# Kernel optimization log

Measured on AMD Instinct MI355X. Metric: run time of the kernel, lower is better.

The kernel has to match this reference:

```python
import jax, jax.numpy as jnp
import numpy as np

B, G, T, F_IN = 32, 128, 128, 318


def _lin(x, W, b):
    # torch Linear: y = x @ W.T + b, W: (out, in)
    return x @ W.T + b


def _sap(rep, W1, b1, W2, b2):
    # SelfAttentionPooling over second-to-last axis. rep: (..., T, H)
    s = _lin(jax.nn.relu(_lin(rep, W1, b1)), W2, b2)[..., 0]  # (..., T)
    w = jax.nn.softmax(s, axis=-1)
    return jnp.einsum('...th,...t->...h', rep, w)  # (..., H)


def setup_inputs() -> dict:
    key = jax.random.key(0)
    ks = jax.random.split(key, 20)

    def w(k, shape, fan_in):
        bound = 1.0 / np.sqrt(fan_in)
        return jax.random.uniform(k, shape, jnp.float32, -bound, bound)

    inp = {
        'x': jax.random.normal(ks[0], (B, G, T, F_IN), jnp.float32),
        # model1: 318->50->20->20
        'W1a': w(ks[1], (50, 318), 318), 'b1a': w(ks[2], (50,), 318),
        'W1b': w(ks[3], (20, 50), 50),  'b1b': w(ks[4], (20,), 50),
        'W1c': w(ks[5], (20, 20), 20),  'b1c': w(ks[6], (20,), 20),
        # model2 pooling (input_dim=20, hidden=10)
        'pW1': w(ks[7], (10, 20), 20),  'pb1': w(ks[8], (10,), 20),
        'pW2': w(ks[9], (1, 10), 10),   'pb2': w(ks[10], (1,), 10),
        # model2_1 pooling
        'qW1': w(ks[11], (10, 20), 20), 'qb1': w(ks[12], (10,), 20),
        'qW2': w(ks[13], (1, 10), 10),  'qb2': w(ks[14], (1,), 10),
        # model3: 20->10->1
        'W3a': w(ks[15], (10, 20), 20), 'b3a': w(ks[16], (10,), 20),
        'W3b': w(ks[17], (1, 10), 10),  'b3b': w(ks[18], (1,), 10),
    }
    return inp


def reference(x, W1a, b1a, W1b, b1b, W1c, b1c, pW1, pb1, pW2, pb2,
              qW1, qb1, qW2, qb2, W3a, b3a, W3b, b3b):
    # model1 MLP on features: (B,G,T,318) -> (B,G,T,20)
    h = jax.nn.relu(_lin(x, W1a, b1a))
    h = jax.nn.relu(_lin(h, W1b, b1b))
    h = jax.nn.relu(_lin(h, W1c, b1c))
    # pool over T: (B,G,20)
    r = _sap(h, pW1, pb1, pW2, pb2)
    # pool over G: (B,20)
    r = _sap(r, qW1, qb1, qW2, qb2)
    # F.normalize (L2 over dim=1, eps=1e-12)
    norm = jnp.linalg.norm(r, axis=-1, keepdims=True)
    r = r / jnp.maximum(norm, 1e-12)
    # model3: (B,1)
    out = _lin(jax.nn.relu(_lin(r, W3a, b3a)), W3b, b3b)
    return out
```

## Files before the change

kernel.cpp:

```cpp
#include <hip/hip_runtime.h>
#include <hip/hip_bf16.h>
#include <math.h>
#include <stdint.h>

typedef __attribute__((ext_vector_type(8))) short bf16x8;
typedef __attribute__((ext_vector_type(4))) float floatx4;

static __device__ __forceinline__ unsigned short f32_to_bf16_rne(float f) {
    union { float f; uint32_t u; } v; v.f = f;
    uint32_t u = v.u;
    return (unsigned short)((u + 0x7fffu + ((u >> 16) & 1u)) >> 16);
}
static __device__ __forceinline__ float bf16_to_f32(unsigned short h) {
    union { uint32_t u; float f; } v; v.u = ((uint32_t)h) << 16;
    return v.f;
}
static __device__ __forceinline__ bf16x8 cvt8(const float2* p) {
    union { __hip_bfloat162 h[4]; bf16x8 v; } u;
    #pragma unroll
    for (int j = 0; j < 4; ++j)
        u.h[j] = __float22bfloat162_rn({p[j].x, p[j].y});
    return u.v;
}

#define BAR() do { \
    asm volatile("s_waitcnt lgkmcnt(0)" ::: "memory"); \
    __builtin_amdgcn_s_barrier(); \
    asm volatile("" ::: "memory"); } while (0)

__global__ void prep_w(const float* __restrict__ W1a, unsigned short* __restrict__ Bpre) {
    int idx = blockIdx.x * 256 + threadIdx.x;
    if (idx >= 40960) return;
    int e  = idx & 7;
    int n  = (idx >> 3) & 63;
    int kq = (idx >> 9) & 3;
    int p  = (idx >> 11) & 1;
    int ks = idx >> 12;
    int k  = ks * 32 + kq * 8 + e;
    float w = (n < 50 && k < 318) ? W1a[n * 318 + k] : 0.0f;
    unsigned short hi = f32_to_bf16_rne(w);
    Bpre[idx] = (p == 0) ? hi : f32_to_bf16_rne(w - bf16_to_f32(hi));
}

#define SLAB (64 * 318)
#define H1S 52

__global__ __launch_bounds__(256, 2)
void gemm_h1(const float* __restrict__ x,
             const unsigned short* __restrict__ Bpre,
             const float* __restrict__ b1a,
             float* __restrict__ h1g)
{
    __shared__ __align__(16) char bsm[81920];

    const int tid  = threadIdx.x;
    const int wv   = tid >> 6;
    const int lane = tid & 63;
    const int fr   = lane & 15;
    const int kq   = lane >> 4;

    const float* arow = x + (size_t)blockIdx.x * SLAB + (wv * 16 + fr) * 318 + kq * 8;

    floatx4 gb[20];
    #pragma unroll
    for (int j = 0; j < 20; ++j)
        gb[j] = *(const floatx4*)((const char*)Bpre + (j * 256 + tid) * 16);

    float2 af[40];
    #pragma unroll
    for (int ks = 0; ks < 10; ++ks)
        #pragma unroll
        for (int j = 0; j < 4; ++j) {
            bool pad = (ks == 9) && (kq == 3) && (j == 3);
            af[ks * 4 + j] = pad ? make_float2(0.f, 0.f)
                                 : *(const float2*)(arow + ks * 32 + 2 * j);
        }
    __builtin_amdgcn_sched_barrier(0);

    #pragma unroll
    for (int j = 0; j < 20; ++j)
        *(floatx4*)(bsm + (j * 256 + tid) * 16) = gb[j];
    BAR();

    floatx4 acc[4];
    #pragma unroll
    for (int nf = 0; nf < 4; ++nf) acc[nf] = (floatx4){0.f, 0.f, 0.f, 0.f};

    #pragma unroll
    for (int ks = 0; ks < 10; ++ks) {
        const char* bb = bsm + ks * 8192 + (kq << 10) + (fr << 4);
        bf16x8 a = cvt8(&af[ks * 4]);
        #pragma unroll
        for (int nf = 0; nf < 4; ++nf) {
            bf16x8 bh = *(const bf16x8*)(bb + nf * 256);
            bf16x8 bl = *(const bf16x8*)(bb + 4096 + nf * 256);
            acc[nf] = __builtin_amdgcn_mfma_f32_16x16x32_bf16(a, bh, acc[nf], 0, 0, 0);
            acc[nf] = __builtin_amdgcn_mfma_f32_16x16x32_bf16(a, bl, acc[nf], 0, 0, 0);
        }
    }

    {
        float* hrow = h1g + ((size_t)blockIdx.x * 64 + wv * 16 + kq * 4) * H1S;
        #pragma unroll
        for (int nf = 0; nf < 4; ++nf) {
            int n = nf * 16 + fr;
            if (n < 50) {
                float bia = b1a[n];
                #pragma unroll
                for (int r = 0; r < 4; ++r)
                    hrow[r * H1S + n] = fmaxf(acc[nf][r] + bia, 0.0f);
            }
        }
    }
}

__global__ __launch_bounds__(256, 4)
void tail_pool(const float* __restrict__ h1g,
               const float* __restrict__ W1b, const float* __restrict__ b1b,
               const float* __restrict__ W1c, const float* __restrict__ b1c,
               const float* __restrict__ pW1, const float* __restrict__ pb1,
               const float* __restrict__ pW2, const float* __restrict__ pb2,
               float* __restrict__ partials)
{
    const int t    = blockIdx.x * 256 + threadIdx.x;
    const int lane = threadIdx.x & 63;

    float hv[52];
    {
        const float4* hr = (const float4*)(h1g + (size_t)t * H1S);
        #pragma unroll
        for (int j = 0; j < 13; ++j) {
            float4 u = hr[j];
            hv[4 * j] = u.x; hv[4 * j + 1] = u.y;
            hv[4 * j + 2] = u.z; hv[4 * j + 3] = u.w;
        }
    }

    float h2[20];
    #pragma unroll
    for (int o = 0; o < 20; ++o) h2[o] = b1b[o];
    #pragma unroll
    for (int i = 0; i < 50; ++i) {
        float hvv = hv[i];
        #pragma unroll
        for (int o = 0; o < 20; ++o) h2[o] = fmaf(hvv, W1b[o * 50 + i], h2[o]);
    }
    #pragma unroll
    for (int o = 0; o < 20; ++o) h2[o] = fmaxf(h2[o], 0.0f);

    float h3[20];
    #pragma unroll
    for (int o = 0; o < 20; ++o) {
        float a = b1c[o];
        const float* w = W1c + o * 20;
        #pragma unroll
        for (int i = 0; i < 20; ++i) a = fmaf(h2[i], w[i], a);
        h3[o] = fmaxf(a, 0.0f);
    }

    float s = pb2[0];
    #pragma unroll
    for (int j = 0; j < 10; ++j) {
        float a = pb1[j];
        const float* w = pW1 + j * 20;
        #pragma unroll
        for (int i = 0; i < 20; ++i) a = fmaf(h3[i], w[i], a);
        s = fmaf(fmaxf(a, 0.0f), pW2[j], s);
    }

    float m = s;
    #pragma unroll
    for (int d = 32; d > 0; d >>= 1) m = fmaxf(m, __shfl_xor(m, d));
    float e = expf(s - m);
    float S = e;
    #pragma unroll
    for (int d = 32; d > 0; d >>= 1) S += __shfl_xor(S, d);

    float V[20];
    #pragma unroll
    for (int o = 0; o < 20; ++o) {
        float v = e * h3[o];
        #pragma unroll
        for (int d = 32; d > 0; d >>= 1) v += __shfl_xor(v, d);
        V[o] = v;
    }

    float myv = m;
    if (lane == 1) myv = S;
    #pragma unroll
    for (int o = 0; o < 20; ++o) if (lane == o + 2) myv = V[o];
    if (lane < 22) partials[(size_t)(t >> 6) * 24 + lane] = myv;
}

__global__ __launch_bounds__(128, 4)
void pool_g_head(const float* __restrict__ partials,
                 const float* __restrict__ qW1, const float* __restrict__ qb1,
                 const float* __restrict__ qW2, const float* __restrict__ qb2,
                 const float* __restrict__ W3a, const float* __restrict__ b3a,
                 const float* __restrict__ W3b, const float* __restrict__ b3b,
                 float* __restrict__ out)
{
    __shared__ float red_m[2];
    __shared__ float red_s[2];
    __shared__ float part[2][20];

    const int tid = threadIdx.x;
    const int b = blockIdx.x;
    const float* P = partials + ((size_t)(b * 128 + tid)) * 48;

    float m0 = P[0], S0 = P[1], m1 = P[24], S1 = P[25];
    float m = fmaxf(m0, m1);
    float w0 = expf(m0 - m), w1 = expf(m1 - m);
    float den = fmaf(S0, w0, S1 * w1);

    float v[20];
    #pragma unroll
    for (int o = 0; o < 20; ++o)
        v[o] = fmaf(P[2 + o], w0, P[26 + o] * w1) / den;

    float s = qb2[0];
    #pragma unroll
    for (int j = 0; j < 10; ++j) {
        float a = qb1[j];
        const float* w = qW1 + j * 20;
        #pragma unroll
        for (int i = 0; i < 20; ++i) a = fmaf(v[i], w[i], a);
        s = fmaf(fmaxf(a, 0.0f), qW2[j], s);
    }

    const int wig = tid >> 6, lane = tid & 63;
    float mm = s;
    #pragma unroll
    for (int d = 32; d > 0; d >>= 1) mm = fmaxf(mm, __shfl_xor(mm, d));
    if (lane == 0) red_m[wig] = mm;
    __syncthreads();
    mm = fmaxf(red_m[0], red_m[1]);

    float e = expf(s - mm);
    float su = e;
    #pragma unroll
    for (int d = 32; d > 0; d >>= 1) su += __shfl_xor(su, d);
    if (lane == 0) red_s[wig] = su;

    #pragma unroll
    for (int o = 0; o < 20; ++o) {
        float val = e * v[o];
        #pragma unroll
        for (int d = 32; d > 0; d >>= 1) val += __shfl_xor(val, d);
        if (lane == 0) part[wig][o] = val;
    }
    __syncthreads();

    if (tid == 0) {
        float dg = red_s[0] + red_s[1];
        float rb[20];
        float n2 = 0.0f;
        #pragma unroll
        for (int o = 0; o < 20; ++o) {
            rb[o] = (part[0][o] + part[1][o]) / dg;
            n2 = fmaf(rb[o], rb[o], n2);
        }
        float nrm = fmaxf(sqrtf(n2), 1e-12f);
        #pragma unroll
        for (int o = 0; o < 20; ++o) rb[o] /= nrm;

        float accv = b3b[0];
        #pragma unroll
        for (int j = 0; j < 10; ++j) {
            float a = b3a[j];
            const float* w = W3a + j * 20;
            #pragma unroll
            for (int i = 0; i < 20; ++i) a = fmaf(rb[i], w[i], a);
            accv = fmaf(fmaxf(a, 0.0f), W3b[j], accv);
        }
        out[b] = accv;
    }
}

extern "C" void kernel_launch(void* const* d_in, const int* in_sizes, int n_in,
                              void* d_out, int out_size, void* d_ws, size_t ws_size,
                              hipStream_t stream) {
    const float* x   = (const float*)d_in[0];
    const float* W1a = (const float*)d_in[1];
    const float* b1a = (const float*)d_in[2];
    const float* W1b = (const float*)d_in[3];
    const float* b1b = (const float*)d_in[4];
    const float* W1c = (const float*)d_in[5];
    const float* b1c = (const float*)d_in[6];
    const float* pW1 = (const float*)d_in[7];
    const float* pb1 = (const float*)d_in[8];
    const float* pW2 = (const float*)d_in[9];
    const float* pb2 = (const float*)d_in[10];
    const float* qW1 = (const float*)d_in[11];
    const float* qb1 = (const float*)d_in[12];
    const float* qW2 = (const float*)d_in[13];
    const float* qb2 = (const float*)d_in[14];
    const float* W3a = (const float*)d_in[15];
    const float* b3a = (const float*)d_in[16];
    const float* W3b = (const float*)d_in[17];
    const float* b3b = (const float*)d_in[18];

    float* partials      = (float*)d_ws;
    unsigned short* Bpre = (unsigned short*)((char*)d_ws + 786432);
    float* h1g           = (float*)((char*)d_ws + 868352);

    prep_w<<<160, 256, 0, stream>>>(W1a, Bpre);
    gemm_h1<<<8192, 256, 0, stream>>>(x, Bpre, b1a, h1g);
    tail_pool<<<2048, 256, 0, stream>>>(
        h1g, W1b, b1b, W1c, b1c, pW1, pb1, pW2, pb2, partials);
    pool_g_head<<<32, 128, 0, stream>>>(
        partials, qW1, qb1, qW2, qb2, W3a, b3a, W3b, b3b, (float*)d_out);
}
```

Measured before the change: 242.9 us.

## Make gemm_h1 persistent over 8 slabs with double-buffered A register prefetch

Each gemm_h1 block now handles 8 consecutive 64-row slabs instead of one, so the B-matrix staging into LDS happens once per 8 slabs. Within the block, the next slab's A tile is loaded into a second register buffer while the current slab is converted to bf16 and multiplied with MFMA, overlapping global loads with compute. A is loaded as float4 and the bias is hoisted into registers. The cost is higher register pressure from two 20-float4 buffers at launch bounds (256,2), and fewer blocks (1024) to spread across the GPU.

```diff
diff --git a/kernel.cpp b/kernel.cpp
--- a/kernel.cpp
+++ b/kernel.cpp
@@ -15,11 +15,12 @@
     union { uint32_t u; float f; } v; v.u = ((uint32_t)h) << 16;
     return v.f;
 }
-static __device__ __forceinline__ bf16x8 cvt8(const float2* p) {
+static __device__ __forceinline__ bf16x8 cvt8(float4 a, float4 b) {
     union { __hip_bfloat162 h[4]; bf16x8 v; } u;
-    #pragma unroll
-    for (int j = 0; j < 4; ++j)
-        u.h[j] = __float22bfloat162_rn({p[j].x, p[j].y});
+    u.h[0] = __float22bfloat162_rn({a.x, a.y});
+    u.h[1] = __float22bfloat162_rn({a.z, a.w});
+    u.h[2] = __float22bfloat162_rn({b.x, b.y});
+    u.h[3] = __float22bfloat162_rn({b.z, b.w});
     return u.v;
 }
 
@@ -45,6 +46,42 @@
 #define SLAB (64 * 318)
 #define H1S 52
 
+#define LOADA(AF, SOFF) { \
+    const float* ap_ = abase0 + (size_t)(SOFF) * SLAB; \
+    _Pragma("unroll") for (int ks_ = 0; ks_ < 10; ++ks_) { \
+        AF[2 * ks_] = *(const float4*)(ap_ + ks_ * 32); \
+        if (ks_ == 9 && kq == 3) { \
+            float2 t_ = *(const float2*)(ap_ + 9 * 32 + 4); \
+            AF[19] = make_float4(t_.x, t_.y, 0.f, 0.f); \
+        } else { \
+            AF[2 * ks_ + 1] = *(const float4*)(ap_ + ks_ * 32 + 4); \
+        } \
+    } } \
+    __builtin_amdgcn_sched_barrier(0);
+
+#define COMPSTORE(AF, SOFF) { \
+    floatx4 acc[4]; \
+    _Pragma("unroll") for (int nf_ = 0; nf_ < 4; ++nf_) \
+        acc[nf_] = (floatx4){0.f, 0.f, 0.f, 0.f}; \
+    _Pragma("unroll") for (int ks_ = 0; ks_ < 10; ++ks_) { \
+        const char* bb_ = bsm + ks_ * 8192 + (kq << 10) + (fr << 4); \
+        bf16x8 a_ = cvt8(AF[2 * ks_], AF[2 * ks_ + 1]); \
+        _Pragma("unroll") for (int nf_ = 0; nf_ < 4; ++nf_) { \
+            bf16x8 bh_ = *(const bf16x8*)(bb_ + nf_ * 256); \
+            bf16x8 bl_ = *(const bf16x8*)(bb_ + 4096 + nf_ * 256); \
+            acc[nf_] = __builtin_amdgcn_mfma_f32_16x16x32_bf16(a_, bh_, acc[nf_], 0, 0, 0); \
+            acc[nf_] = __builtin_amdgcn_mfma_f32_16x16x32_bf16(a_, bl_, acc[nf_], 0, 0, 0); \
+        } \
+    } \
+    float* hrow_ = h1g + ((slab0 + (SOFF)) * 64 + wv * 16 + kq * 4) * H1S; \
+    _Pragma("unroll") for (int nf_ = 0; nf_ < 4; ++nf_) { \
+        int n_ = nf_ * 16 + fr; \
+        if (n_ < 50) { \
+            _Pragma("unroll") for (int r_ = 0; r_ < 4; ++r_) \
+                hrow_[r_ * H1S + n_] = fmaxf(acc[nf_][r_] + bia4[nf_], 0.0f); \
+        } \
+    } }
+
 __global__ __launch_bounds__(256, 2)
 void gemm_h1(const float* __restrict__ x,
              const unsigned short* __restrict__ Bpre,
@@ -59,58 +96,36 @@
     const int fr   = lane & 15;
     const int kq   = lane >> 4;
 
-    const float* arow = x + (size_t)blockIdx.x * SLAB + (wv * 16 + fr) * 318 + kq * 8;
+    const size_t slab0 = (size_t)blockIdx.x * 8;
+    const float* abase0 = x + slab0 * SLAB + (wv * 16 + fr) * 318 + kq * 8;
 
     floatx4 gb[20];
     #pragma unroll
     for (int j = 0; j < 20; ++j)
         gb[j] = *(const floatx4*)((const char*)Bpre + (j * 256 + tid) * 16);
 
-    float2 af[40];
-    #pragma unroll
-    for (int ks = 0; ks < 10; ++ks)
-        #pragma unroll
-        for (int j = 0; j < 4; ++j) {
-            bool pad = (ks == 9) && (kq == 3) && (j == 3);
-            af[ks * 4 + j] = pad ? make_float2(0.f, 0.f)
-                                 : *(const float2*)(arow + ks * 32 + 2 * j);
-        }
-    __builtin_amdgcn_sched_barrier(0);
+    float4 af0[20], af1[20];
+    LOADA(af0, 0);
+
+    float bia4[4];
+    #pragma unroll
+    for (int nf = 0; nf < 4; ++nf) {
+        int n = nf * 16 + fr;
+        bia4[nf] = (n < 50) ? b1a[n] : 0.0f;
+    }
 
     #pragma unroll
     for (int j = 0; j < 20; ++j)
         *(floatx4*)(bsm + (j * 256 + tid) * 16) = gb[j];
     BAR();
 
-    floatx4 acc[4];
-    #pragma unroll
-    for (int nf = 0; nf < 4; ++nf) acc[nf] = (floatx4){0.f, 0.f, 0.f, 0.f};
-
-    #pragma unroll
-    for (int ks = 0; ks < 10; ++ks) {
-        const char* bb = bsm + ks * 8192 + (kq << 10) + (fr << 4);
-        bf16x8 a = cvt8(&af[ks * 4]);
-        #pragma unroll
-        for (int nf = 0; nf < 4; ++nf) {
-            bf16x8 bh = *(const bf16x8*)(bb + nf * 256);
-            bf16x8 bl = *(const bf16x8*)(bb + 4096 + nf * 256);
-            acc[nf] = __builtin_amdgcn_mfma_f32_16x16x32_bf16(a, bh, acc[nf], 0, 0, 0);
-            acc[nf] = __builtin_amdgcn_mfma_f32_16x16x32_bf16(a, bl, acc[nf], 0, 0, 0);
-        }
-    }
-
-    {
-        float* hrow = h1g + ((size_t)blockIdx.x * 64 + wv * 16 + kq * 4) * H1S;
-        #pragma unroll
-        for (int nf = 0; nf < 4; ++nf) {
-            int n = nf * 16 + fr;
-            if (n < 50) {
-                float bia = b1a[n];
-                #pragma unroll
-                for (int r = 0; r < 4; ++r)
-                    hrow[r * H1S + n] = fmaxf(acc[nf][r] + bia, 0.0f);
-            }
-        }
+    #pragma unroll 1
+    for (int p = 0; p < 4; ++p) {
+        const int s = 2 * p;
+        LOADA(af1, s + 1);
+        COMPSTORE(af0, s);
+        if (p < 3) { LOADA(af0, s + 2); }
+        COMPSTORE(af1, s + 1);
     }
 }
 
@@ -305,7 +320,7 @@
     float* h1g           = (float*)((char*)d_ws + 868352);
 
     prep_w<<<160, 256, 0, stream>>>(W1a, Bpre);
-    gemm_h1<<<8192, 256, 0, stream>>>(x, Bpre, b1a, h1g);
+    gemm_h1<<<1024, 256, 0, stream>>>(x, Bpre, b1a, h1g);
     tail_pool<<<2048, 256, 0, stream>>>(
         h1g, W1b, b1b, W1c, b1c, pW1, pb1, pW2, pb2, partials);
     pool_g_head<<<32, 128, 0, stream>>>(
```

After: 252.5 us. +4.0%, slower.

## Pipeline x slab via async global-to-LDS loads and keep W1a fragments in registers

Applied to the files above, without the earlier changes.

The first-layer GEMM now keeps each wave's B fragments (hi/lo bf16 split) in registers and has each wave own one 16-column output tile. It no longer stages all of W1a in LDS. The 64-row x slab is streamed in four 16-row quarters through a double-buffered LDS ring filled by global_load_lds, so loads overlap with MFMA compute. LDS use shrinks and launch bounds go from 2 to 3 blocks per CU to raise occupancy. The trade-offs are more barriers, a hardcoded clamp on the end-of-buffer address, and possible LDS bank conflicts from the 1272-byte row stride.

```diff
diff --git a/kernel.cpp b/kernel.cpp
--- a/kernel.cpp
+++ b/kernel.cpp
@@ -15,18 +15,14 @@
     union { uint32_t u; float f; } v; v.u = ((uint32_t)h) << 16;
     return v.f;
 }
-static __device__ __forceinline__ bf16x8 cvt8(const float2* p) {
+static __device__ __forceinline__ bf16x8 cvt8(floatx4 a, floatx4 b) {
     union { __hip_bfloat162 h[4]; bf16x8 v; } u;
-    #pragma unroll
-    for (int j = 0; j < 4; ++j)
-        u.h[j] = __float22bfloat162_rn({p[j].x, p[j].y});
+    u.h[0] = __float22bfloat162_rn({a[0], a[1]});
+    u.h[1] = __float22bfloat162_rn({a[2], a[3]});
+    u.h[2] = __float22bfloat162_rn({b[0], b[1]});
+    u.h[3] = __float22bfloat162_rn({b[2], b[3]});
     return u.v;
 }
-
-#define BAR() do { \
-    asm volatile("s_waitcnt lgkmcnt(0)" ::: "memory"); \
-    __builtin_amdgcn_s_barrier(); \
-    asm volatile("" ::: "memory"); } while (0)
 
 __global__ void prep_w(const float* __restrict__ W1a, unsigned short* __restrict__ Bpre) {
     int idx = blockIdx.x * 256 + threadIdx.x;
@@ -42,16 +38,22 @@
     Bpre[idx] = (p == 0) ? hi : f32_to_bf16_rne(w - bf16_to_f32(hi));
 }
 
-#define SLAB (64 * 318)
-#define H1S 52
-
-__global__ __launch_bounds__(256, 2)
+#define SLABB 81408
+#define QDATA 20352
+#define QSTG  20480
+#define H1S   52
+
+#define GLL(g, l) __builtin_amdgcn_global_load_lds( \
+    (const __attribute__((address_space(1))) void*)(g), \
+    (__attribute__((address_space(3))) void*)(l), 16, 0, 0)
+
+__global__ __launch_bounds__(256, 3)
 void gemm_h1(const float* __restrict__ x,
              const unsigned short* __restrict__ Bpre,
              const float* __restrict__ b1a,
              float* __restrict__ h1g)
 {
-    __shared__ __align__(16) char bsm[81920];
+    __shared__ __align__(1024) char sbuf[2 * QSTG];
 
     const int tid  = threadIdx.x;
     const int wv   = tid >> 6;
@@ -59,59 +61,71 @@
     const int fr   = lane & 15;
     const int kq   = lane >> 4;
 
-    const float* arow = x + (size_t)blockIdx.x * SLAB + (wv * 16 + fr) * 318 + kq * 8;
-
-    floatx4 gb[20];
-    #pragma unroll
-    for (int j = 0; j < 20; ++j)
-        gb[j] = *(const floatx4*)((const char*)Bpre + (j * 256 + tid) * 16);
-
-    float2 af[40];
-    #pragma unroll
-    for (int ks = 0; ks < 10; ++ks)
-        #pragma unroll
-        for (int j = 0; j < 4; ++j) {
-            bool pad = (ks == 9) && (kq == 3) && (j == 3);
-            af[ks * 4 + j] = pad ? make_float2(0.f, 0.f)
-                                 : *(const float2*)(arow + ks * 32 + 2 * j);
+    const size_t slab = blockIdx.x;
+    const char* xs = (const char*)x + slab * SLABB;
+    const char* xclamp = (const char*)x + 666894336 - 16;
+
+    bf16x8 Bh[10], Bl[10];
+    {
+        const char* bb = (const char*)Bpre + (kq << 10) + ((wv * 16 + fr) << 4);
+        #pragma unroll
+        for (int ks = 0; ks < 10; ++ks) {
+            Bh[ks] = *(const bf16x8*)(bb + ks * 8192);
+            Bl[ks] = *(const bf16x8*)(bb + ks * 8192 + 4096);
         }
-    __builtin_amdgcn_sched_barrier(0);
-
-    #pragma unroll
-    for (int j = 0; j < 20; ++j)
-        *(floatx4*)(bsm + (j * 256 + tid) * 16) = gb[j];
-    BAR();
-
-    floatx4 acc[4];
-    #pragma unroll
-    for (int nf = 0; nf < 4; ++nf) acc[nf] = (floatx4){0.f, 0.f, 0.f, 0.f};
-
-    #pragma unroll
-    for (int ks = 0; ks < 10; ++ks) {
-        const char* bb = bsm + ks * 8192 + (kq << 10) + (fr << 4);
-        bf16x8 a = cvt8(&af[ks * 4]);
-        #pragma unroll
-        for (int nf = 0; nf < 4; ++nf) {
-            bf16x8 bh = *(const bf16x8*)(bb + nf * 256);
-            bf16x8 bl = *(const bf16x8*)(bb + 4096 + nf * 256);
-            acc[nf] = __builtin_amdgcn_mfma_f32_16x16x32_bf16(a, bh, acc[nf], 0, 0, 0);
-            acc[nf] = __builtin_amdgcn_mfma_f32_16x16x32_bf16(a, bl, acc[nf], 0, 0, 0);
-        }
-    }
-
-    {
-        float* hrow = h1g + ((size_t)blockIdx.x * 64 + wv * 16 + kq * 4) * H1S;
-        #pragma unroll
-        for (int nf = 0; nf < 4; ++nf) {
-            int n = nf * 16 + fr;
-            if (n < 50) {
-                float bia = b1a[n];
-                #pragma unroll
-                for (int r = 0; r < 4; ++r)
-                    hrow[r * H1S + n] = fmaxf(acc[nf][r] + bia, 0.0f);
-            }
-        }
-    }
+    }
+    const int n = wv * 16 + fr;
+    const float bia = (n < 50) ? b1a[n] : 0.0f;
+
+#define STAGE(b, q) { \
+    char* lb = sbuf + (b) * QSTG + wv * 1024; \
+    const char* gs = xs + (size_t)(q) * QDATA + wv * 1024 + lane * 16; \
+    _Pragma("unroll") for (int j = 0; j < 5; ++j) { \
+        const char* g = gs + j * 4096; \
+        if (g > xclamp) g = xclamp; \
+        GLL(g, lb + j * 4096); \
+    } }
+
+#define WAITBAR(NSTR) do { \
+    asm volatile("s_waitcnt vmcnt(" NSTR ")" ::: "memory"); \
+    __builtin_amdgcn_s_barrier(); \
+    __builtin_amdgcn_sched_barrier(0); } while (0)
+
+#define COMPUTE(b, q) { \
+    floatx4 acc = (floatx4){0.f, 0.f, 0.f, 0.f}; \
+    const char* ab = sbuf + (b) * QSTG + fr * 1272 + kq * 32; \
+    _Pragma("unroll") for (int ks = 0; ks < 10; ++ks) { \
+        floatx4 lo = *(const floatx4*)(ab + ks * 128); \
+        floatx4 hi = *(const floatx4*)(ab + ks * 128 + 16); \
+        bf16x8 a = cvt8(lo, hi); \
+        acc = __builtin_amdgcn_mfma_f32_16x16x32_bf16(a, Bh[ks], acc, 0, 0, 0); \
+        acc = __builtin_amdgcn_mfma_f32_16x16x32_bf16(a, Bl[ks], acc, 0, 0, 0); \
+    } \
+    if (n < 50) { \
+        float* hrow = h1g + ((slab * 64 + (q) * 16 + kq * 4) * H1S) + n; \
+        _Pragma("unroll") for (int r = 0; r < 4; ++r) \
+            hrow[r * H1S] = fmaxf(acc[r] + bia, 0.0f); \
+    } }
+
+    STAGE(0, 0);
+    WAITBAR("0");
+
+    STAGE(1, 1);
+    COMPUTE(0, 0);
+
+    WAITBAR("4");
+    STAGE(0, 2);
+    COMPUTE(1, 1);
+
+    WAITBAR("4");
+    STAGE(1, 3);
+    COMPUTE(0, 2);
+
+    WAITBAR("4");
+    COMPUTE(1, 3);
+#undef STAGE
+#undef WAITBAR
+#undef COMPUTE
 }
 
 __global__ __launch_bounds__(256, 4)
```

Result: slower. 364.2 us (+49.9%).
